# Performance work log

Measured on AMD Instinct MI355X. Metric: run time of the kernel, lower is better.

## Reference

```python
import jax, jax.numpy as jnp
import numpy as np

LN_EPS = 1e-5

def _mlp3(x, w1, b1, w2, b2, g, bt, w3, b3):
    # Linear -> ReLU -> Linear -> LayerNorm -> ReLU -> Linear
    h = jax.nn.relu(x @ w1 + b1)
    h = h @ w2 + b2
    mu = jnp.mean(h, axis=-1, keepdims=True)
    var = jnp.mean(jnp.square(h - mu), axis=-1, keepdims=True)
    h = g * (h - mu) * jax.lax.rsqrt(var + LN_EPS) + bt
    h = jax.nn.relu(h)
    return h @ w3 + b3

def _edge_index(B, n):
    # fully connected incl. self-loops, row-major (i, j) per graph, batch-offset
    ij = jnp.arange(n * n)
    i = ij // n
    j = ij % n
    off = (jnp.arange(B) * n)[:, None]
    row = (off + i[None, :]).reshape(-1)  # [B*n*n]
    col = (off + j[None, :]).reshape(-1)
    return row, col

def setup_inputs() -> dict:
    key = jax.random.key(0)
    ks = jax.random.split(key, 16)
    D, H = 512, 512
    B, n = 4096, 7
    s = 0.02
    inp = {
        'states': jax.random.normal(ks[0], (B, n, D), jnp.float32),
        'ew1': jax.random.normal(ks[1], (2 * D, H)) * s, 'eb1': jnp.zeros((H,)),
        'ew2': jax.random.normal(ks[2], (H, H)) * s, 'eb2': jnp.zeros((H,)),
        'eg': jnp.ones((H,)), 'ebt': jnp.zeros((H,)),
        'ew3': jax.random.normal(ks[3], (H, H)) * s, 'eb3': jnp.zeros((H,)),
        'nw1': jax.random.normal(ks[4], (D + H, H)) * s, 'nb1': jnp.zeros((H,)),
        'nw2': jax.random.normal(ks[5], (H, H)) * s, 'nb2': jnp.zeros((H,)),
        'ng': jnp.ones((H,)), 'nbt': jnp.zeros((H,)),
        'nw3': jax.random.normal(ks[6], (H, H)) * s, 'nb3': jnp.zeros((H,)),
        'fnw': jax.random.normal(ks[7], (H, 1)) * s, 'fnb': jnp.zeros((1,)),
        'few': jax.random.normal(ks[8], (H, 1)) * s, 'feb': jnp.zeros((1,)),
    }
    return inp

def reference(states, ew1, eb1, ew2, eb2, eg, ebt, ew3, eb3,
              nw1, nb1, nw2, nb2, ng, nbt, nw3, nb3, fnw, fnb, few, feb):
    B, n, D = states.shape
    node = states.reshape(-1, D)                       # [B*n, D]
    row, col = _edge_index(B, n)                       # [B*n*n]

    def edge_mlp(src, tgt):
        return _mlp3(jnp.concatenate([src, tgt], axis=1),
                     ew1, eb1, ew2, eb2, eg, ebt, ew3, eb3)

    edge_attr = edge_mlp(node[row], node[col])         # [B*n*n, H]
    agg = jax.ops.segment_sum(edge_attr, row, num_segments=B * n)
    node2 = _mlp3(jnp.concatenate([node, agg], axis=1),
                  nw1, nb1, nw2, nb2, ng, nbt, nw3, nb3)
    edge_attr2 = edge_mlp(node2[row], node2[col])

    node_out = (node2 @ fnw + fnb).reshape(B, n)       # unary_preds=1
    edge_out = (edge_attr2 @ few + feb).reshape(B, n * n)
    return jnp.concatenate([node_out, edge_out], axis=1)  # [B, n + n*n]
```

## Files before the change

### kernel.cpp

```cpp
#include <hip/hip_runtime.h>

#define LN_EPS 1e-5f

typedef unsigned short u16;
typedef u16 u16x8 __attribute__((ext_vector_type(8)));
typedef __bf16 bf16x8 __attribute__((ext_vector_type(8)));
typedef float f32x4 __attribute__((ext_vector_type(4)));
typedef float f32x2 __attribute__((ext_vector_type(2)));

__device__ __forceinline__ u16 f2bf(float f){
  return __builtin_bit_cast(u16, (__bf16)f);
}
__device__ __forceinline__ float bf2f(u16 b){
  return (float)__builtin_bit_cast(__bf16, b);
}
__device__ __forceinline__ f32x4 mfma16(u16x8 a, u16x8 b, f32x4 c){
  return __builtin_amdgcn_mfma_f32_16x16x32_bf16(
      __builtin_bit_cast(bf16x8, a), __builtin_bit_cast(bf16x8, b), c, 0, 0, 0);
}
__device__ __forceinline__ int uidx(int row, int k){
  return row * 512 + (k ^ ((row & 7) << 3));
}

__device__ __forceinline__ void zero_acc(f32x4 (&acc)[4][4]){
  #pragma unroll
  for (int mt = 0; mt < 4; ++mt)
    #pragma unroll
    for (int ct = 0; ct < 4; ++ct){
      f32x4 z = {0.f, 0.f, 0.f, 0.f};
      acc[mt][ct] = z;
    }
}

__device__ __forceinline__ void preload_b4(const u16* __restrict__ Bp, int wave, int lane,
                                           u16x8 (&b)[4]){
  const u16* bb = Bp + ((size_t)(wave * 4) * 64 + lane) * 8;
  #pragma unroll
  for (int ct = 0; ct < 4; ++ct) b[ct] = *(const u16x8*)&bb[ct * 512];
}

__device__ __forceinline__ void gemm_pipe(const u16* hA, const u16* __restrict__ Bp,
                                          f32x4 (&acc)[4][4], int wave, int lane,
                                          u16x8 (&b_cur)[4]){
  int lrow = lane & 15, lhi = lane >> 4;
  const u16* bb = Bp + ((size_t)(wave * 4) * 64 + lane) * 8;
  u16x8 b_nxt[4], a[4];
  #pragma unroll
  for (int kt = 0; kt < 16; ++kt){
    #pragma unroll
    for (int mt = 0; mt < 4; ++mt)
      a[mt] = *(const u16x8*)&hA[uidx(mt * 16 + lrow, kt * 32 + lhi * 8)];
    if (kt < 15){
      #pragma unroll
      for (int ct = 0; ct < 4; ++ct)
        b_nxt[ct] = *(const u16x8*)&bb[(size_t)(kt + 1) * 16384 + ct * 512];
    }
    __builtin_amdgcn_s_setprio(1);
    #pragma unroll
    for (int ct = 0; ct < 4; ++ct)
      #pragma unroll
      for (int mt = 0; mt < 4; ++mt)
        acc[mt][ct] = mfma16(a[mt], b_cur[ct], acc[mt][ct]);
    __builtin_amdgcn_s_setprio(0);
    #pragma unroll
    for (int ct = 0; ct < 4; ++ct) b_cur[ct] = b_nxt[ct];
  }
}

__device__ __forceinline__ void gemm_k1024_gA(const u16* __restrict__ A0,
                                              const u16* __restrict__ A1, size_t row0,
                                              const u16* __restrict__ Bp,
                                              f32x4 (&acc)[4][4], int wave, int lane){
  int lrow = lane & 15, lhi = lane >> 4;
  const u16* bb = Bp + ((size_t)(wave * 4) * 64 + lane) * 8;
  const u16* a0 = A0 + (row0 + lrow) * 512 + lhi * 8;
  const u16* a1 = A1 + (row0 + lrow) * 512 + lhi * 8;
  u16x8 b_cur[4], b_nxt[4], a[4];
  #pragma unroll
  for (int ct = 0; ct < 4; ++ct) b_cur[ct] = *(const u16x8*)&bb[ct * 512];
  #pragma unroll
  for (int kt = 0; kt < 32; ++kt){
    const u16* ab = (kt < 16) ? a0 : a1;
    int kk = (kt & 15) * 32;
    #pragma unroll
    for (int mt = 0; mt < 4; ++mt)
      a[mt] = *(const u16x8*)&ab[mt * 8192 + kk];
    if (kt < 31){
      #pragma unroll
      for (int ct = 0; ct < 4; ++ct)
        b_nxt[ct] = *(const u16x8*)&bb[(size_t)(kt + 1) * 16384 + ct * 512];
    }
    __builtin_amdgcn_s_setprio(1);
    #pragma unroll
    for (int ct = 0; ct < 4; ++ct)
      #pragma unroll
      for (int mt = 0; mt < 4; ++mt)
        acc[mt][ct] = mfma16(a[mt], b_cur[ct], acc[mt][ct]);
    __builtin_amdgcn_s_setprio(0);
    #pragma unroll
    for (int ct = 0; ct < 4; ++ct) b_cur[ct] = b_nxt[ct];
  }
}

__device__ __forceinline__ void gemm_pipe_s(const u16* hA, const u16* __restrict__ bbBase,
                                            int ktStride, f32x4 (&acc)[4][4],
                                            int lane){
  int lrow = lane & 15, lhi = lane >> 4;
  u16x8 b_cur[4], b_nxt[4], a[4];
  #pragma unroll
  for (int ct = 0; ct < 4; ++ct) b_cur[ct] = *(const u16x8*)&bbBase[ct * 512];
  #pragma unroll
  for (int kt = 0; kt < 16; ++kt){
    #pragma unroll
    for (int mt = 0; mt < 4; ++mt)
      a[mt] = *(const u16x8*)&hA[uidx(mt * 16 + lrow, kt * 32 + lhi * 8)];
    if (kt < 15){
      #pragma unroll
      for (int ct = 0; ct < 4; ++ct)
        b_nxt[ct] = *(const u16x8*)&bbBase[(size_t)(kt + 1) * ktStride + ct * 512];
    }
    __builtin_amdgcn_s_setprio(1);
    #pragma unroll
    for (int ct = 0; ct < 4; ++ct)
      #pragma unroll
      for (int mt = 0; mt < 4; ++mt)
        acc[mt][ct] = mfma16(a[mt], b_cur[ct], acc[mt][ct]);
    __builtin_amdgcn_s_setprio(0);
    #pragma unroll
    for (int ct = 0; ct < 4; ++ct) b_cur[ct] = b_nxt[ct];
  }
}

__device__ __forceinline__ void add_bias8(f32x4 (&acc)[4][4], const float* __restrict__ b,
                                          int wave, int lane){
  int lrow = lane & 15;
  #pragma unroll
  for (int ct = 0; ct < 4; ++ct){
    float bb = b[wave * 64 + ct * 16 + lrow];
    #pragma unroll
    for (int mt = 0; mt < 4; ++mt)
      #pragma unroll
      for (int r = 0; r < 4; ++r) acc[mt][ct][r] += bb;
  }
}

__device__ __forceinline__ void relu_to_lds(f32x4 (&acc)[4][4], u16* hA,
                                            const float* __restrict__ b,
                                            int wave, int lane){
  int lrow = lane & 15, lhi = lane >> 4;
  #pragma unroll
  for (int ct = 0; ct < 4; ++ct){
    int c = wave * 64 + ct * 16 + lrow;
    float bb = b[c];
    #pragma unroll
    for (int mt = 0; mt < 4; ++mt)
      #pragma unroll
      for (int r = 0; r < 4; ++r){
        int row = mt * 16 + lhi * 4 + r;
        hA[uidx(row, c)] = f2bf(fmaxf(acc[mt][ct][r] + bb, 0.f));
      }
  }
}

template<int TO_ACC>
__device__ __forceinline__ void ln_relu8_t(f32x4 (&acc)[4][4], u16* hA,
    f32x2 (*stats)[8], f32x2* mufb,
    const float* __restrict__ b2, const float* __restrict__ g, const float* __restrict__ bt,
    int wave, int lane, int tid)
{
  int lrow = lane & 15, lhi = lane >> 4;
  float s1[4][4], s2[4][4];
  #pragma unroll
  for (int mt = 0; mt < 4; ++mt)
    #pragma unroll
    for (int r = 0; r < 4; ++r){ s1[mt][r] = 0.f; s2[mt][r] = 0.f; }
  #pragma unroll
  for (int ct = 0; ct < 4; ++ct){
    int c = wave * 64 + ct * 16 + lrow;
    float bb = b2[c];
    #pragma unroll
    for (int mt = 0; mt < 4; ++mt)
      #pragma unroll
      for (int r = 0; r < 4; ++r){
        float x = acc[mt][ct][r] + bb;
        acc[mt][ct][r] = x;
        s1[mt][r] += x; s2[mt][r] += x * x;
      }
  }
  #pragma unroll
  for (int off = 1; off < 16; off <<= 1){
    #pragma unroll
    for (int mt = 0; mt < 4; ++mt)
      #pragma unroll
      for (int r = 0; r < 4; ++r){
        s1[mt][r] += __shfl_xor(s1[mt][r], off);
        s2[mt][r] += __shfl_xor(s2[mt][r], off);
      }
  }
  float sa1 = 0.f, sa2 = 0.f;
  #pragma unroll
  for (int mt = 0; mt < 4; ++mt)
    #pragma unroll
    for (int r = 0; r < 4; ++r)
      if (lrow == mt * 4 + r){ sa1 = s1[mt][r]; sa2 = s2[mt][r]; }
  int rowa = (lrow >> 2) * 16 + lhi * 4 + (lrow & 3);
  f32x2 pa = {sa1, sa2};
  stats[rowa][wave] = pa;
  __syncthreads();
  if (tid < 64){
    float a = 0.f, b = 0.f;
    #pragma unroll
    for (int w = 0; w < 8; ++w){ a += stats[tid][w][0]; b += stats[tid][w][1]; }
    float mu  = a * (1.f / 512.f);
    float var = b * (1.f / 512.f) - mu * mu;
    f32x2 mr = {mu, rsqrtf(fmaxf(var, 0.f) + LN_EPS)};
    mufb[tid] = mr;
  }
  __syncthreads();
  float gv[4], btv[4];
  #pragma unroll
  for (int ct = 0; ct < 4; ++ct){
    int c = wave * 64 + ct * 16 + lrow;
    gv[ct] = g[c]; btv[ct] = bt[c];
  }
  #pragma unroll
  for (int mt = 0; mt < 4; ++mt)
    #pragma unroll
    for (int r = 0; r < 4; ++r){
      int row = mt * 16 + lhi * 4 + r;
      f32x2 mr = mufb[row];
      #pragma unroll
      for (int ct = 0; ct < 4; ++ct){
        int c = wave * 64 + ct * 16 + lrow;
        float x = (acc[mt][ct][r] - mr[0]) * mr[1] * gv[ct] + btv[ct];
        if (TO_ACC) acc[mt][ct][r] = fmaxf(x, 0.f);
        else        hA[uidx(row, c)] = f2bf(fmaxf(x, 0.f));
      }
    }
}

__device__ __forceinline__ void head_partial8(f32x4 (&acc)[4][4], const float* __restrict__ w,
                                              f32x2 (*stats)[8], int wave, int lane)
{
  int lrow = lane & 15, lhi = lane >> 4;
  float hs[4][4];
  #pragma unroll
  for (int mt = 0; mt < 4; ++mt)
    #pragma unroll
    for (int r = 0; r < 4; ++r) hs[mt][r] = 0.f;
  #pragma unroll
  for (int ct = 0; ct < 4; ++ct){
    int c = wave * 64 + ct * 16 + lrow;
    float f = w[c];
    #pragma unroll
    for (int mt = 0; mt < 4; ++mt)
      #pragma unroll
      for (int r = 0; r < 4; ++r) hs[mt][r] += acc[mt][ct][r] * f;
  }
  #pragma unroll
  for (int off = 1; off < 16; off <<= 1)
    #pragma unroll
    for (int mt = 0; mt < 4; ++mt)
      #pragma unroll
      for (int r = 0; r < 4; ++r) hs[mt][r] += __shfl_xor(hs[mt][r], off);
  float sa = 0.f;
  #pragma unroll
  for (int mt = 0; mt < 4; ++mt)
    #pragma unroll
    for (int r = 0; r < 4; ++r)
      if (lrow == mt * 4 + r) sa = hs[mt][r];
  int rowa = (lrow >> 2) * 16 + lhi * 4 + (lrow & 3);
  f32x2 pa = {sa, 0.f};
  stats[rowa][wave] = pa;
}

__device__ __forceinline__ void stage_h1(const u16* __restrict__ PQ, int gg, u16* hA,
                                         const float* bias, int wave, int lane){
  const u16* Pg = PQ + (size_t)gg * 7 * 1024;
  u16x8 pA, qA, pB, qB;
  {
    int e = wave;
    int i = e / 7, j = e % 7;
    pA = *(const u16x8*)&Pg[(size_t)i * 1024 + lane * 8];
    qA = *(const u16x8*)&Pg[(size_t)j * 1024 + 512 + lane * 8];
  }
  #pragma unroll
  for (int it = 0; it < 8; ++it){
    int e = it * 8 + wave;
    if (it < 7){
      int e2 = e + 8;
      if (e2 < 49){
        int i = e2 / 7, j = e2 % 7;
        pB = *(const u16x8*)&Pg[(size_t)i * 1024 + lane * 8];
        qB = *(const u16x8*)&Pg[(size_t)j * 1024 + 512 + lane * 8];
      }
    }
    u16x8 o;
    if (e < 49){
      #pragma unroll
      for (int u = 0; u < 8; ++u)
        o[u] = f2bf(fmaxf(bf2f(pA[u]) + bf2f(qA[u]) + bias[u], 0.f));
    } else {
      #pragma unroll
      for (int u = 0; u < 8; ++u) o[u] = 0;
    }
    *(u16x8*)&hA[uidx(e, lane * 8)] = o;
    pA = pB; qA = qB;
  }
}

__global__ __launch_bounds__(512, 2) void edge0_kernel(
    const u16* __restrict__ PQ, const u16* __restrict__ w2p,
    const float* __restrict__ b1, const float* __restrict__ b2,
    const float* __restrict__ g, const float* __restrict__ bt,
    u16* __restrict__ hsum)
{
  __shared__ alignas(16) u16 hA[64 * 512];
  __shared__ f32x2 stats[64][8];
  __shared__ f32x2 mufb[64];
  int gidx = blockIdx.x;
  int tid = threadIdx.x;
  int wave = tid >> 6, lane = tid & 63;

  const float4* b1v = (const float4*)b1;
  float4 ba = b1v[lane * 2], bb2 = b1v[lane * 2 + 1];
  float bias[8] = {ba.x, ba.y, ba.z, ba.w, bb2.x, bb2.y, bb2.z, bb2.w};

  stage_h1(PQ, gidx, hA, bias, wave, lane);
  u16x8 bpre[4];
  preload_b4(w2p, wave, lane, bpre);
  __syncthreads();

  f32x4 acc[4][4];
  zero_acc(acc);
  gemm_pipe(hA, w2p, acc, wave, lane, bpre);
  ln_relu8_t<0>(acc, hA, stats, mufb, b2, g, bt, wave, lane, tid);
  __syncthreads();
  {
    int c = tid;
    #pragma unroll
    for (int i = 0; i < 7; ++i){
      float s = 0.f;
      #pragma unroll
      for (int j = 0; j < 7; ++j)
        s += bf2f(hA[uidx(7 * i + j, c)]);
      hsum[((size_t)(gidx * 7 + i)) * 512 + c] = f2bf(s);
    }
  }
}

__global__ __launch_bounds__(512, 2) void edge1_kernel(
    const u16* __restrict__ PQ, const u16* __restrict__ w2p,
    const float* __restrict__ b1, const float* __restrict__ b2,
    const float* __restrict__ g, const float* __restrict__ bt,
    const float* __restrict__ w3f, float* __restrict__ out)
{
  __shared__ alignas(16) u16 hA[64 * 512];
  __shared__ f32x2 stats[64][8];
  __shared__ f32x2 mufb[64];
  int gidx = blockIdx.x;
  int tid = threadIdx.x;
  int wave = tid >> 6, lane = tid & 63;

  const float4* b1v = (const float4*)b1;
  float4 ba = b1v[lane * 2], bb2 = b1v[lane * 2 + 1];
  float bias[8] = {ba.x, ba.y, ba.z, ba.w, bb2.x, bb2.y, bb2.z, bb2.w};

  stage_h1(PQ, gidx, hA, bias, wave, lane);
  u16x8 bpre[4];
  preload_b4(w2p, wave, lane, bpre);
  __syncthreads();

  f32x4 acc[4][4];
  zero_acc(acc);
  gemm_pipe(hA, w2p, acc, wave, lane, bpre);
  ln_relu8_t<1>(acc, hA, stats, mufb, b2, g, bt, wave, lane, tid);
  head_partial8(acc, w3f, stats, wave, lane);
  __syncthreads();
  if (tid < 49){
    float s = w3f[512];
    #pragma unroll
    for (int w = 0; w < 8; ++w) s += stats[tid][w][0];
    out[(size_t)gidx * 56 + 7 + tid] = s;
  }
}

__global__ __launch_bounds__(512, 2) void node_mega(
    const u16* __restrict__ nodeb, const u16* __restrict__ hsumb,
    const u16* __restrict__ nw1cat, const u16* __restrict__ nw2p,
    const u16* __restrict__ nw3p, const u16* __restrict__ w1p,
    const float* __restrict__ bvec, const float* __restrict__ nb2,
    const float* __restrict__ ng, const float* __restrict__ nbt,
    const float* __restrict__ nb3, const float* __restrict__ hw,
    const float* __restrict__ hb,
    u16* __restrict__ PQ, float* __restrict__ out)
{
  __shared__ alignas(16) u16 hA[64 * 512];
  __shared__ f32x2 stats[64][8];
  __shared__ f32x2 mufb[64];
  int tid = threadIdx.x;
  int wave = tid >> 6, lane = tid & 63;
  int lrow = lane & 15, lhi = lane >> 4;
  size_t row0 = (size_t)blockIdx.x * 64;

  f32x4 acc[4][4];
  zero_acc(acc);
  gemm_k1024_gA(nodeb, hsumb, row0, nw1cat, acc, wave, lane);
  relu_to_lds(acc, hA, bvec, wave, lane);
  u16x8 bpre[4];
  preload_b4(nw2p, wave, lane, bpre);
  __syncthreads();
  zero_acc(acc);
  gemm_pipe(hA, nw2p, acc, wave, lane, bpre);
  ln_relu8_t<0>(acc, hA, stats, mufb, nb2, ng, nbt, wave, lane, tid);
  preload_b4(nw3p, wave, lane, bpre);
  __syncthreads();
  zero_acc(acc);
  gemm_pipe(hA, nw3p, acc, wave, lane, bpre);
  add_bias8(acc, nb3, wave, lane);
  __syncthreads();
  #pragma unroll
  for (int ct = 0; ct < 4; ++ct){
    int c = wave * 64 + ct * 16 + lrow;
    #pragma unroll
    for (int mt = 0; mt < 4; ++mt)
      #pragma unroll
      for (int r = 0; r < 4; ++r)
        hA[uidx(mt * 16 + lhi * 4 + r, c)] = f2bf(acc[mt][ct][r]);
  }
  head_partial8(acc, hw, stats, wave, lane);
  __syncthreads();
  if (tid < 64){
    size_t v = row0 + tid;
    float s = hb[0];
    #pragma unroll
    for (int w = 0; w < 8; ++w) s += stats[tid][w][0];
    out[(v / 7) * 56 + (v % 7)] = s;
  }
  #pragma unroll
  for (int p = 0; p < 2; ++p){
    zero_acc(acc);
    const u16* bbBase = w1p + (((size_t)(p * 32) + wave * 4) * 64 + lane) * 8;
    gemm_pipe_s(hA, bbBase, 32768, acc, lane);
    #pragma unroll
    for (int ct = 0; ct < 4; ++ct){
      int c = p * 512 + wave * 64 + ct * 16 + lrow;
      #pragma unroll
      for (int mt = 0; mt < 4; ++mt)
        #pragma unroll
        for (int r = 0; r < 4; ++r){
          size_t grow = row0 + mt * 16 + lhi * 4 + r;
          PQ[grow * 1024 + c] = f2bf(acc[mt][ct][r]);
        }
    }
  }
}

__global__ __launch_bounds__(256, 2) void gemm64_0(
    const u16* __restrict__ A0, const u16* __restrict__ Bp, u16* __restrict__ Cout)
{
  int tid = threadIdx.x;
  int wave = tid >> 6, lane = tid & 63;
  int lrow = lane & 15, lhi = lane >> 4;
  size_t row0 = (size_t)blockIdx.x * 64;
  int coff = blockIdx.y * 512;
  const u16* bb = Bp + (((size_t)(coff >> 4) + wave * 8) * 64 + lane) * 8;
  f32x4 acc[4][8];
  #pragma unroll
  for (int mt = 0; mt < 4; ++mt)
    #pragma unroll
    for (int ct = 0; ct < 8; ++ct){
      f32x4 z = {0.f, 0.f, 0.f, 0.f};
      acc[mt][ct] = z;
    }
  u16x8 b_cur[8], b_nxt[8];
  #pragma unroll
  for (int ct = 0; ct < 8; ++ct) b_cur[ct] = *(const u16x8*)&bb[ct * 512];
  #pragma unroll
  for (int kt = 0; kt < 16; ++kt){
    u16x8 af[4];
    #pragma unroll
    for (int mt = 0; mt < 4; ++mt)
      af[mt] = *(const u16x8*)&A0[(row0 + mt * 16 + lrow) * 512 + kt * 32 + lhi * 8];
    if (kt < 15){
      #pragma unroll
      for (int ct = 0; ct < 8; ++ct)
        b_nxt[ct] = *(const u16x8*)&bb[((size_t)(kt + 1) * 64 * 64 + ct * 64) * 8];
    }
    __builtin_amdgcn_s_setprio(1);
    #pragma unroll
    for (int ct = 0; ct < 8; ++ct)
      #pragma unroll
      for (int mt = 0; mt < 4; ++mt) acc[mt][ct] = mfma16(af[mt], b_cur[ct], acc[mt][ct]);
    __builtin_amdgcn_s_setprio(0);
    #pragma unroll
    for (int ct = 0; ct < 8; ++ct) b_cur[ct] = b_nxt[ct];
  }
  #pragma unroll
  for (int ct = 0; ct < 8; ++ct){
    int c = coff + wave * 128 + ct * 16 + lrow;
    #pragma unroll
    for (int mt = 0; mt < 4; ++mt)
      #pragma unroll
      for (int r = 0; r < 4; ++r){
        size_t grow = row0 + mt * 16 + lhi * 4 + r;
        Cout[grow * 1024 + c] = f2bf(acc[mt][ct][r]);
      }
  }
}

__global__ __launch_bounds__(256) void gemm_w3n(
    const float* __restrict__ A, const u16* __restrict__ Bp, float* __restrict__ C)
{
  int tid = threadIdx.x;
  int wave = tid >> 6, lane = tid & 63;
  int lrow = lane & 15, lhi = lane >> 4;
  size_t row0 = (size_t)blockIdx.x * 64;
  const u16* bb = Bp + (((size_t)(wave * 8)) * 64 + lane) * 8;
  f32x4 acc[4][8];
  #pragma unroll
  for (int mt = 0; mt < 4; ++mt)
    #pragma unroll
    for (int ct = 0; ct < 8; ++ct){
      f32x4 z = {0.f, 0.f, 0.f, 0.f};
      acc[mt][ct] = z;
    }
  for (int kt = 0; kt < 16; ++kt){
    u16x8 af[4], bv[8];
    #pragma unroll
    for (int mt = 0; mt < 4; ++mt){
      const float* ar = A + (row0 + mt * 16 + lrow) * 512 + kt * 32 + lhi * 8;
      float4 v0 = *(const float4*)ar, v1 = *(const float4*)(ar + 4);
      af[mt][0] = f2bf(v0.x); af[mt][1] = f2bf(v0.y);
      af[mt][2] = f2bf(v0.z); af[mt][3] = f2bf(v0.w);
      af[mt][4] = f2bf(v1.x); af[mt][5] = f2bf(v1.y);
      af[mt][6] = f2bf(v1.z); af[mt][7] = f2bf(v1.w);
    }
    #pragma unroll
    for (int ct = 0; ct < 8; ++ct)
      bv[ct] = *(const u16x8*)&bb[(size_t)kt * 16384 + ct * 512];
    #pragma unroll
    for (int ct = 0; ct < 8; ++ct)
      #pragma unroll
      for (int mt = 0; mt < 4; ++mt) acc[mt][ct] = mfma16(af[mt], bv[ct], acc[mt][ct]);
  }
  #pragma unroll
  for (int ct = 0; ct < 8; ++ct){
    int c = wave * 128 + ct * 16 + lrow;
    #pragma unroll
    for (int mt = 0; mt < 4; ++mt)
      #pragma unroll
      for (int r = 0; r < 4; ++r){
        size_t grow = row0 + mt * 16 + lhi * 4 + r;
        C[grow * 512 + c] = acc[mt][ct][r];
      }
  }
}

__global__ void fold_bvec(const float* __restrict__ nb1, const float* __restrict__ b3,
                          const float* __restrict__ nw1, float* __restrict__ bvec)
{
  int c = threadIdx.x;
  float s = 0.f;
  for (int m = 0; m < 512; ++m)
    s += b3[m] * nw1[(size_t)(512 + m) * 512 + c];
  bvec[c] = nb1[c] + 7.f * s;
}

__global__ void fold_w3(const float* __restrict__ W3, const float* __restrict__ hw,
                        const float* __restrict__ b3, const float* __restrict__ hb,
                        float* __restrict__ w3f)
{
  int k = blockIdx.x, l = threadIdx.x;
  const float* row = (k < 512) ? (W3 + (size_t)k * 512) : b3;
  float s = 0.f;
  for (int c = l; c < 512; c += 64) s += row[c] * hw[c];
  #pragma unroll
  for (int off = 32; off; off >>= 1) s += __shfl_down(s, off);
  if (l == 0) w3f[k] = (k < 512) ? s : s + hb[0];
}

__global__ void pack_w(const float* __restrict__ W, u16* __restrict__ dst,
                       int K, int N, int w1mode)
{
  int idx = blockIdx.x * 256 + threadIdx.x;
  int total = (K >> 5) * (N >> 4) * 64;
  if (idx >= total) return;
  int lane = idx & 63;
  int t = idx >> 6;
  int nt = N >> 4;
  int ct = t % nt;
  int kt = t / nt;
  int c  = ct * 16 + (lane & 15);
  int k0 = kt * 32 + (lane >> 4) * 8;
  u16x8 o;
  #pragma unroll
  for (int j = 0; j < 8; ++j){
    int k = k0 + j;
    float v;
    if (w1mode){
      v = (c < 512) ? W[(size_t)k * 512 + c] : W[(size_t)(k + 512) * 512 + (c - 512)];
    } else {
      v = W[(size_t)k * N + c];
    }
    o[j] = f2bf(v);
  }
  *(u16x8*)&dst[(size_t)idx * 8] = o;
}

__global__ void cast_node(const float* __restrict__ src, u16* __restrict__ dst, int n8){
  int idx = blockIdx.x * 256 + threadIdx.x;
  if (idx >= n8) return;
  const float4* s = (const float4*)src;
  float4 a = s[(size_t)idx * 2], b = s[(size_t)idx * 2 + 1];
  u16x8 o;
  o[0] = f2bf(a.x); o[1] = f2bf(a.y); o[2] = f2bf(a.z); o[3] = f2bf(a.w);
  o[4] = f2bf(b.x); o[5] = f2bf(b.y); o[6] = f2bf(b.z); o[7] = f2bf(b.w);
  *(u16x8*)&dst[(size_t)idx * 8] = o;
}

extern "C" void kernel_launch(void* const* d_in, const int* in_sizes, int n_in,
                              void* d_out, int out_size, void* d_ws, size_t ws_size,
                              hipStream_t stream)
{
  (void)in_sizes; (void)n_in; (void)out_size; (void)ws_size;
  const float* states = (const float*)d_in[0];
  const float* ew1 = (const float*)d_in[1];
  const float* eb1 = (const float*)d_in[2];
  const float* ew2 = (const float*)d_in[3];
  const float* eb2 = (const float*)d_in[4];
  const float* eg  = (const float*)d_in[5];
  const float* ebt = (const float*)d_in[6];
  const float* ew3 = (const float*)d_in[7];
  const float* eb3 = (const float*)d_in[8];
  const float* nw1 = (const float*)d_in[9];
  const float* nb1 = (const float*)d_in[10];
  const float* nw2 = (const float*)d_in[11];
  const float* nb2 = (const float*)d_in[12];
  const float* ng  = (const float*)d_in[13];
  const float* nbt = (const float*)d_in[14];
  const float* nw3 = (const float*)d_in[15];
  const float* nb3 = (const float*)d_in[16];
  const float* fnw = (const float*)d_in[17];
  const float* fnb = (const float*)d_in[18];
  const float* few = (const float*)d_in[19];
  const float* feb = (const float*)d_in[20];
  float* out = (float*)d_out;

  char* ws = (char*)d_ws;
  size_t off = 0;
  auto alloc = [&](size_t bytes) -> void* {
    void* p = ws + off;
    off += (bytes + 255) & ~(size_t)255;
    return p;
  };
  const size_t NV = 28672;
  u16* PQ     = (u16*)alloc(NV * 1024 * 2);
  u16* nodeb  = (u16*)alloc(NV * 512 * 2);
  u16* hsumb  = (u16*)alloc(NV * 512 * 2);
  u16* w1p    = (u16*)alloc(512 * 1024 * 2);
  u16* nw1cat = (u16*)alloc(1024 * 512 * 2);
  u16* nw1bp  = (u16*)alloc(512 * 512 * 2);
  u16* w2p    = (u16*)alloc(512 * 512 * 2);
  u16* nw2p   = (u16*)alloc(512 * 512 * 2);
  u16* nw3p   = (u16*)alloc(512 * 512 * 2);
  float* w3n  = (float*)alloc(512 * 512 * 4);
  float* w3f  = (float*)alloc(513 * 4);
  float* bvec = (float*)alloc(512 * 4);

  pack_w<<<256, 256, 0, stream>>>(ew1, w1p, 512, 1024, 1);
  pack_w<<<128, 256, 0, stream>>>(nw1, nw1cat, 512, 512, 0);
  pack_w<<<128, 256, 0, stream>>>(nw1 + 512 * 512, nw1bp, 512, 512, 0);
  pack_w<<<128, 256, 0, stream>>>(ew2, w2p, 512, 512, 0);
  pack_w<<<128, 256, 0, stream>>>(nw2, nw2p, 512, 512, 0);
  pack_w<<<128, 256, 0, stream>>>(nw3, nw3p, 512, 512, 0);
  fold_w3<<<513, 64, 0, stream>>>(ew3, few, eb3, feb, w3f);
  fold_bvec<<<1, 512, 0, stream>>>(nb1, eb3, nw1, bvec);
  gemm_w3n<<<8, 256, 0, stream>>>(ew3, nw1bp, w3n);
  pack_w<<<128, 256, 0, stream>>>(w3n, nw1cat + 512 * 512, 512, 512, 0);
  cast_node<<<7168, 256, 0, stream>>>(states, nodeb, (int)(NV * 512 / 8));

  gemm64_0<<<dim3(448, 2), 256, 0, stream>>>(nodeb, w1p, PQ);
  edge0_kernel<<<4096, 512, 0, stream>>>(PQ, w2p, eb1, eb2, eg, ebt, hsumb);
  node_mega<<<448, 512, 0, stream>>>(nodeb, hsumb, nw1cat, nw2p, nw3p, w1p,
                                     bvec, nb2, ng, nbt, nb3, fnw, fnb, PQ, out);
  edge1_kernel<<<4096, 512, 0, stream>>>(PQ, w2p, eb1, eb2, eg, ebt, w3f, out);
}
```

Baseline: 580.3 us.

## Fold edge bias into P, use transpose-reduce shuffles, fuse head dot, widen setup grids

Adds the first edge-layer bias to the P half when P/Q are written, so the per-edge staging no longer adds it for each of the 49 edges. Replaces the 16-value butterfly shuffle reductions with a recursive-halving transpose reduction that needs 15 shuffles instead of 64, using bit-reversed row indexing. Fuses the LayerNorm, ReLU and head dot product in edge1 and in the node head so the activations are not written back into the accumulator before the dot. Spreads fold_bvec and gemm_w3n over more blocks to cut setup latency. The reordered reduction changes floating-point summation order slightly.

```diff
diff --git a/kernel.cpp b/kernel.cpp
--- a/kernel.cpp
+++ b/kernel.cpp
@@ -21,6 +21,9 @@
 __device__ __forceinline__ int uidx(int row, int k){
   return row * 512 + (k ^ ((row & 7) << 3));
 }
+__device__ __forceinline__ int bitrev4(int l){
+  return ((l & 1) << 3) | ((l & 2) << 1) | ((l & 4) >> 1) | ((l & 8) >> 3);
+}
 
 __device__ __forceinline__ void zero_acc(f32x4 (&acc)[4][4]){
   #pragma unroll
@@ -30,6 +33,20 @@
       f32x4 z = {0.f, 0.f, 0.f, 0.f};
       acc[mt][ct] = z;
     }
+}
+
+__device__ __forceinline__ float reduce16(float (&x)[16], int lrow){
+  #pragma unroll
+  for (int b = 1; b < 16; b <<= 1){
+    const int h = 8 / b;
+    #pragma unroll
+    for (int k = 0; k < h; ++k){
+      float mine  = (lrow & b) ? x[k + h] : x[k];
+      float other = (lrow & b) ? x[k] : x[k + h];
+      x[k] = mine + __shfl_xor(other, b);
+    }
+  }
+  return x[0];
 }
 
 __device__ __forceinline__ void preload_b4(const u16* __restrict__ Bp, int wave, int lane,
@@ -162,18 +179,14 @@
   }
 }
 
-template<int TO_ACC>
-__device__ __forceinline__ void ln_relu8_t(f32x4 (&acc)[4][4], u16* hA,
-    f32x2 (*stats)[8], f32x2* mufb,
-    const float* __restrict__ b2, const float* __restrict__ g, const float* __restrict__ bt,
+__device__ __forceinline__ void ln_stats(f32x4 (&acc)[4][4],
+    f32x2 (*stats)[8], f32x2* mufb, const float* __restrict__ b2,
     int wave, int lane, int tid)
 {
   int lrow = lane & 15, lhi = lane >> 4;
-  float s1[4][4], s2[4][4];
-  #pragma unroll
-  for (int mt = 0; mt < 4; ++mt)
-    #pragma unroll
-    for (int r = 0; r < 4; ++r){ s1[mt][r] = 0.f; s2[mt][r] = 0.f; }
+  float s1[16], s2[16];
+  #pragma unroll
+  for (int p = 0; p < 16; ++p){ s1[p] = 0.f; s2[p] = 0.f; }
   #pragma unroll
   for (int ct = 0; ct < 4; ++ct){
     int c = wave * 64 + ct * 16 + lrow;
@@ -184,27 +197,26 @@
       for (int r = 0; r < 4; ++r){
         float x = acc[mt][ct][r] + bb;
         acc[mt][ct][r] = x;
-        s1[mt][r] += x; s2[mt][r] += x * x;
+        s1[mt * 4 + r] += x;
+        s2[mt * 4 + r] += x * x;
       }
   }
   #pragma unroll
-  for (int off = 1; off < 16; off <<= 1){
-    #pragma unroll
-    for (int mt = 0; mt < 4; ++mt)
-      #pragma unroll
-      for (int r = 0; r < 4; ++r){
-        s1[mt][r] += __shfl_xor(s1[mt][r], off);
-        s2[mt][r] += __shfl_xor(s2[mt][r], off);
-      }
-  }
-  float sa1 = 0.f, sa2 = 0.f;
-  #pragma unroll
-  for (int mt = 0; mt < 4; ++mt)
-    #pragma unroll
-    for (int r = 0; r < 4; ++r)
-      if (lrow == mt * 4 + r){ sa1 = s1[mt][r]; sa2 = s2[mt][r]; }
-  int rowa = (lrow >> 2) * 16 + lhi * 4 + (lrow & 3);
-  f32x2 pa = {sa1, sa2};
+  for (int b = 1; b < 16; b <<= 1){
+    const int h = 8 / b;
+    #pragma unroll
+    for (int k = 0; k < h; ++k){
+      float m1 = (lrow & b) ? s1[k + h] : s1[k];
+      float o1 = (lrow & b) ? s1[k] : s1[k + h];
+      s1[k] = m1 + __shfl_xor(o1, b);
+      float m2 = (lrow & b) ? s2[k + h] : s2[k];
+      float o2 = (lrow & b) ? s2[k] : s2[k + h];
+      s2[k] = m2 + __shfl_xor(o2, b);
+    }
+  }
+  int p = bitrev4(lrow);
+  int rowa = (p >> 2) * 16 + lhi * 4 + (p & 3);
+  f32x2 pa = {s1[0], s2[0]};
   stats[rowa][wave] = pa;
   __syncthreads();
   if (tid < 64){
@@ -217,6 +229,13 @@
     mufb[tid] = mr;
   }
   __syncthreads();
+}
+
+__device__ __forceinline__ void ln_norm_to_lds(f32x4 (&acc)[4][4], u16* hA,
+    f32x2* mufb, const float* __restrict__ g, const float* __restrict__ bt,
+    int wave, int lane)
+{
+  int lrow = lane & 15, lhi = lane >> 4;
   float gv[4], btv[4];
   #pragma unroll
   for (int ct = 0; ct < 4; ++ct){
@@ -233,49 +252,13 @@
       for (int ct = 0; ct < 4; ++ct){
         int c = wave * 64 + ct * 16 + lrow;
         float x = (acc[mt][ct][r] - mr[0]) * mr[1] * gv[ct] + btv[ct];
-        if (TO_ACC) acc[mt][ct][r] = fmaxf(x, 0.f);
-        else        hA[uidx(row, c)] = f2bf(fmaxf(x, 0.f));
+        hA[uidx(row, c)] = f2bf(fmaxf(x, 0.f));
       }
     }
 }
 
-__device__ __forceinline__ void head_partial8(f32x4 (&acc)[4][4], const float* __restrict__ w,
-                                              f32x2 (*stats)[8], int wave, int lane)
-{
-  int lrow = lane & 15, lhi = lane >> 4;
-  float hs[4][4];
-  #pragma unroll
-  for (int mt = 0; mt < 4; ++mt)
-    #pragma unroll
-    for (int r = 0; r < 4; ++r) hs[mt][r] = 0.f;
-  #pragma unroll
-  for (int ct = 0; ct < 4; ++ct){
-    int c = wave * 64 + ct * 16 + lrow;
-    float f = w[c];
-    #pragma unroll
-    for (int mt = 0; mt < 4; ++mt)
-      #pragma unroll
-      for (int r = 0; r < 4; ++r) hs[mt][r] += acc[mt][ct][r] * f;
-  }
-  #pragma unroll
-  for (int off = 1; off < 16; off <<= 1)
-    #pragma unroll
-    for (int mt = 0; mt < 4; ++mt)
-      #pragma unroll
-      for (int r = 0; r < 4; ++r) hs[mt][r] += __shfl_xor(hs[mt][r], off);
-  float sa = 0.f;
-  #pragma unroll
-  for (int mt = 0; mt < 4; ++mt)
-    #pragma unroll
-    for (int r = 0; r < 4; ++r)
-      if (lrow == mt * 4 + r) sa = hs[mt][r];
-  int rowa = (lrow >> 2) * 16 + lhi * 4 + (lrow & 3);
-  f32x2 pa = {sa, 0.f};
-  stats[rowa][wave] = pa;
-}
-
 __device__ __forceinline__ void stage_h1(const u16* __restrict__ PQ, int gg, u16* hA,
-                                         const float* bias, int wave, int lane){
+                                         int wave, int lane){
   const u16* Pg = PQ + (size_t)gg * 7 * 1024;
   u16x8 pA, qA, pB, qB;
   {
@@ -299,7 +282,7 @@
     if (e < 49){
       #pragma unroll
       for (int u = 0; u < 8; ++u)
-        o[u] = f2bf(fmaxf(bf2f(pA[u]) + bf2f(qA[u]) + bias[u], 0.f));
+        o[u] = f2bf(fmaxf(bf2f(pA[u]) + bf2f(qA[u]), 0.f));
     } else {
       #pragma unroll
       for (int u = 0; u < 8; ++u) o[u] = 0;
@@ -311,7 +294,7 @@
 
 __global__ __launch_bounds__(512, 2) void edge0_kernel(
     const u16* __restrict__ PQ, const u16* __restrict__ w2p,
-    const float* __restrict__ b1, const float* __restrict__ b2,
+    const float* __restrict__ b2,
     const float* __restrict__ g, const float* __restrict__ bt,
     u16* __restrict__ hsum)
 {
@@ -322,11 +305,7 @@
   int tid = threadIdx.x;
   int wave = tid >> 6, lane = tid & 63;
 
-  const float4* b1v = (const float4*)b1;
-  float4 ba = b1v[lane * 2], bb2 = b1v[lane * 2 + 1];
-  float bias[8] = {ba.x, ba.y, ba.z, ba.w, bb2.x, bb2.y, bb2.z, bb2.w};
-
-  stage_h1(PQ, gidx, hA, bias, wave, lane);
+  stage_h1(PQ, gidx, hA, wave, lane);
   u16x8 bpre[4];
   preload_b4(w2p, wave, lane, bpre);
   __syncthreads();
@@ -334,7 +313,8 @@
   f32x4 acc[4][4];
   zero_acc(acc);
   gemm_pipe(hA, w2p, acc, wave, lane, bpre);
-  ln_relu8_t<0>(acc, hA, stats, mufb, b2, g, bt, wave, lane, tid);
+  ln_stats(acc, stats, mufb, b2, wave, lane, tid);
+  ln_norm_to_lds(acc, hA, mufb, g, bt, wave, lane);
   __syncthreads();
   {
     int c = tid;
@@ -351,7 +331,7 @@
 
 __global__ __launch_bounds__(512, 2) void edge1_kernel(
     const u16* __restrict__ PQ, const u16* __restrict__ w2p,
-    const float* __restrict__ b1, const float* __restrict__ b2,
+    const float* __restrict__ b2,
     const float* __restrict__ g, const float* __restrict__ bt,
     const float* __restrict__ w3f, float* __restrict__ out)
 {
@@ -361,12 +341,9 @@
   int gidx = blockIdx.x;
   int tid = threadIdx.x;
   int wave = tid >> 6, lane = tid & 63;
-
-  const float4* b1v = (const float4*)b1;
-  float4 ba = b1v[lane * 2], bb2 = b1v[lane * 2 + 1];
-  float bias[8] = {ba.x, ba.y, ba.z, ba.w, bb2.x, bb2.y, bb2.z, bb2.w};
-
-  stage_h1(PQ, gidx, hA, bias, wave, lane);
+  int lrow = lane & 15, lhi = lane >> 4;
+
+  stage_h1(PQ, gidx, hA, wave, lane);
   u16x8 bpre[4];
   preload_b4(w2p, wave, lane, bpre);
   __syncthreads();
@@ -374,8 +351,33 @@
   f32x4 acc[4][4];
   zero_acc(acc);
   gemm_pipe(hA, w2p, acc, wave, lane, bpre);
-  ln_relu8_t<1>(acc, hA, stats, mufb, b2, g, bt, wave, lane, tid);
-  head_partial8(acc, w3f, stats, wave, lane);
+  ln_stats(acc, stats, mufb, b2, wave, lane, tid);
+  float gv[4], btv[4], wv[4];
+  #pragma unroll
+  for (int ct = 0; ct < 4; ++ct){
+    int c = wave * 64 + ct * 16 + lrow;
+    gv[ct] = g[c]; btv[ct] = bt[c]; wv[ct] = w3f[c];
+  }
+  float hs[16];
+  #pragma unroll
+  for (int p = 0; p < 16; ++p) hs[p] = 0.f;
+  #pragma unroll
+  for (int mt = 0; mt < 4; ++mt)
+    #pragma unroll
+    for (int r = 0; r < 4; ++r){
+      int row = mt * 16 + lhi * 4 + r;
+      f32x2 mr = mufb[row];
+      #pragma unroll
+      for (int ct = 0; ct < 4; ++ct){
+        float x = (acc[mt][ct][r] - mr[0]) * mr[1] * gv[ct] + btv[ct];
+        hs[mt * 4 + r] = fmaf(fmaxf(x, 0.f), wv[ct], hs[mt * 4 + r]);
+      }
+    }
+  float sa = reduce16(hs, lrow);
+  int p = bitrev4(lrow);
+  int rowa = (p >> 2) * 16 + lhi * 4 + (p & 3);
+  f32x2 pa = {sa, 0.f};
+  stats[rowa][wave] = pa;
   __syncthreads();
   if (tid < 49){
     float s = w3f[512];
@@ -392,7 +394,7 @@
     const float* __restrict__ bvec, const float* __restrict__ nb2,
     const float* __restrict__ ng, const float* __restrict__ nbt,
     const float* __restrict__ nb3, const float* __restrict__ hw,
-    const float* __restrict__ hb,
+    const float* __restrict__ hb, const float* __restrict__ b1,
     u16* __restrict__ PQ, float* __restrict__ out)
 {
   __shared__ alignas(16) u16 hA[64 * 512];
@@ -412,23 +414,37 @@
   __syncthreads();
   zero_acc(acc);
   gemm_pipe(hA, nw2p, acc, wave, lane, bpre);
-  ln_relu8_t<0>(acc, hA, stats, mufb, nb2, ng, nbt, wave, lane, tid);
+  ln_stats(acc, stats, mufb, nb2, wave, lane, tid);
+  ln_norm_to_lds(acc, hA, mufb, ng, nbt, wave, lane);
   preload_b4(nw3p, wave, lane, bpre);
   __syncthreads();
   zero_acc(acc);
   gemm_pipe(hA, nw3p, acc, wave, lane, bpre);
   add_bias8(acc, nb3, wave, lane);
   __syncthreads();
+  float hs[16];
+  #pragma unroll
+  for (int p = 0; p < 16; ++p) hs[p] = 0.f;
+  float wv[4];
+  #pragma unroll
+  for (int ct = 0; ct < 4; ++ct) wv[ct] = hw[wave * 64 + ct * 16 + lrow];
   #pragma unroll
   for (int ct = 0; ct < 4; ++ct){
     int c = wave * 64 + ct * 16 + lrow;
     #pragma unroll
     for (int mt = 0; mt < 4; ++mt)
       #pragma unroll
-      for (int r = 0; r < 4; ++r)
-        hA[uidx(mt * 16 + lhi * 4 + r, c)] = f2bf(acc[mt][ct][r]);
-  }
-  head_partial8(acc, hw, stats, wave, lane);
+      for (int r = 0; r < 4; ++r){
+        float v = acc[mt][ct][r];
+        hA[uidx(mt * 16 + lhi * 4 + r, c)] = f2bf(v);
+        hs[mt * 4 + r] = fmaf(v, wv[ct], hs[mt * 4 + r]);
+      }
+  }
+  float sa = reduce16(hs, lrow);
+  int p4 = bitrev4(lrow);
+  int rowa = (p4 >> 2) * 16 + lhi * 4 + (p4 & 3);
+  f32x2 pa = {sa, 0.f};
+  stats[rowa][wave] = pa;
   __syncthreads();
   if (tid < 64){
     size_t v = row0 + tid;
@@ -438,26 +454,29 @@
     out[(v / 7) * 56 + (v % 7)] = s;
   }
   #pragma unroll
-  for (int p = 0; p < 2; ++p){
+  for (int pp = 0; pp < 2; ++pp){
     zero_acc(acc);
-    const u16* bbBase = w1p + (((size_t)(p * 32) + wave * 4) * 64 + lane) * 8;
+    const u16* bbBase = w1p + (((size_t)(pp * 32) + wave * 4) * 64 + lane) * 8;
     gemm_pipe_s(hA, bbBase, 32768, acc, lane);
     #pragma unroll
     for (int ct = 0; ct < 4; ++ct){
-      int c = p * 512 + wave * 64 + ct * 16 + lrow;
+      int cc = wave * 64 + ct * 16 + lrow;
+      int c = pp * 512 + cc;
+      float bb = (pp == 0) ? b1[cc] : 0.f;
       #pragma unroll
       for (int mt = 0; mt < 4; ++mt)
         #pragma unroll
         for (int r = 0; r < 4; ++r){
           size_t grow = row0 + mt * 16 + lhi * 4 + r;
-          PQ[grow * 1024 + c] = f2bf(acc[mt][ct][r]);
+          PQ[grow * 1024 + c] = f2bf(acc[mt][ct][r] + bb);
         }
     }
   }
 }
 
 __global__ __launch_bounds__(256, 2) void gemm64_0(
-    const u16* __restrict__ A0, const u16* __restrict__ Bp, u16* __restrict__ Cout)
+    const u16* __restrict__ A0, const u16* __restrict__ Bp,
+    const float* __restrict__ b1, u16* __restrict__ Cout)
 {
   int tid = threadIdx.x;
   int wave = tid >> 6, lane = tid & 63;
@@ -498,13 +517,15 @@
   }
   #pragma unroll
   for (int ct = 0; ct < 8; ++ct){
-    int c = coff + wave * 128 + ct * 16 + lrow;
+    int cc = wave * 128 + ct * 16 + lrow;
+    int c = coff + cc;
+    float bb2 = (coff == 0) ? b1[cc] : 0.f;
     #pragma unroll
     for (int mt = 0; mt < 4; ++mt)
       #pragma unroll
       for (int r = 0; r < 4; ++r){
         size_t grow = row0 + mt * 16 + lhi * 4 + r;
-        Cout[grow * 1024 + c] = f2bf(acc[mt][ct][r]);
+        Cout[grow * 1024 + c] = f2bf(acc[mt][ct][r] + bb2);
       }
   }
 }
@@ -516,17 +537,18 @@
   int wave = tid >> 6, lane = tid & 63;
   int lrow = lane & 15, lhi = lane >> 4;
   size_t row0 = (size_t)blockIdx.x * 64;
-  const u16* bb = Bp + (((size_t)(wave * 8)) * 64 + lane) * 8;
-  f32x4 acc[4][8];
+  int coff = blockIdx.y * 128;
+  const u16* bb = Bp + (((size_t)(coff >> 4) + wave * 2) * 64 + lane) * 8;
+  f32x4 acc[4][2];
   #pragma unroll
   for (int mt = 0; mt < 4; ++mt)
     #pragma unroll
-    for (int ct = 0; ct < 8; ++ct){
+    for (int ct = 0; ct < 2; ++ct){
       f32x4 z = {0.f, 0.f, 0.f, 0.f};
       acc[mt][ct] = z;
     }
   for (int kt = 0; kt < 16; ++kt){
-    u16x8 af[4], bv[8];
+    u16x8 af[4], bv[2];
     #pragma unroll
     for (int mt = 0; mt < 4; ++mt){
       const float* ar = A + (row0 + mt * 16 + lrow) * 512 + kt * 32 + lhi * 8;
@@ -537,16 +559,16 @@
       af[mt][6] = f2bf(v1.z); af[mt][7] = f2bf(v1.w);
     }
     #pragma unroll
-    for (int ct = 0; ct < 8; ++ct)
+    for (int ct = 0; ct < 2; ++ct)
       bv[ct] = *(const u16x8*)&bb[(size_t)kt * 16384 + ct * 512];
     #pragma unroll
-    for (int ct = 0; ct < 8; ++ct)
+    for (int ct = 0; ct < 2; ++ct)
       #pragma unroll
       for (int mt = 0; mt < 4; ++mt) acc[mt][ct] = mfma16(af[mt], bv[ct], acc[mt][ct]);
   }
   #pragma unroll
-  for (int ct = 0; ct < 8; ++ct){
-    int c = wave * 128 + ct * 16 + lrow;
+  for (int ct = 0; ct < 2; ++ct){
+    int c = coff + wave * 32 + ct * 16 + lrow;
     #pragma unroll
     for (int mt = 0; mt < 4; ++mt)
       #pragma unroll
@@ -560,7 +582,7 @@
 __global__ void fold_bvec(const float* __restrict__ nb1, const float* __restrict__ b3,
                           const float* __restrict__ nw1, float* __restrict__ bvec)
 {
-  int c = threadIdx.x;
+  int c = blockIdx.x * 64 + threadIdx.x;
   float s = 0.f;
   for (int m = 0; m < 512; ++m)
     s += b3[m] * nw1[(size_t)(512 + m) * 512 + c];
@@ -675,14 +697,14 @@
   pack_w<<<128, 256, 0, stream>>>(nw2, nw2p, 512, 512, 0);
   pack_w<<<128, 256, 0, stream>>>(nw3, nw3p, 512, 512, 0);
   fold_w3<<<513, 64, 0, stream>>>(ew3, few, eb3, feb, w3f);
-  fold_bvec<<<1, 512, 0, stream>>>(nb1, eb3, nw1, bvec);
-  gemm_w3n<<<8, 256, 0, stream>>>(ew3, nw1bp, w3n);
+  fold_bvec<<<8, 64, 0, stream>>>(nb1, eb3, nw1, bvec);
+  gemm_w3n<<<dim3(8, 4), 256, 0, stream>>>(ew3, nw1bp, w3n);
   pack_w<<<128, 256, 0, stream>>>(w3n, nw1cat + 512 * 512, 512, 512, 0);
   cast_node<<<7168, 256, 0, stream>>>(states, nodeb, (int)(NV * 512 / 8));
 
-  gemm64_0<<<dim3(448, 2), 256, 0, stream>>>(nodeb, w1p, PQ);
-  edge0_kernel<<<4096, 512, 0, stream>>>(PQ, w2p, eb1, eb2, eg, ebt, hsumb);
+  gemm64_0<<<dim3(448, 2), 256, 0, stream>>>(nodeb, w1p, eb1, PQ);
+  edge0_kernel<<<4096, 512, 0, stream>>>(PQ, w2p, eb2, eg, ebt, hsumb);
   node_mega<<<448, 512, 0, stream>>>(nodeb, hsumb, nw1cat, nw2p, nw3p, w1p,
-                                     bvec, nb2, ng, nbt, nb3, fnw, fnb, PQ, out);
-  edge1_kernel<<<4096, 512, 0, stream>>>(PQ, w2p, eb1, eb2, eg, ebt, w3f, out);
-}
+                                     bvec, nb2, ng, nbt, nb3, fnw, fnb, eb1, PQ, out);
+  edge1_kernel<<<4096, 512, 0, stream>>>(PQ, w2p, eb2, eg, ebt, w3f, out);
+}
```

Result: slower. 777.4 us (+34.0%).
